# Kernel tuning notes

Measured on AMD Instinct MI355X. Metric: run time of the kernel, lower is better.

The kernel has to match this reference:

```python
import jax, jax.numpy as jnp
import numpy as np
import math

B, S, D, H, FF, L = 8, 1024, 1024, 8, 4096, 2
DK = D // H
NEG = -1e32
EPS = 1e-5


def _cosine_pe(seq_len, d_model):
    pos = jnp.arange(seq_len, dtype=jnp.float32)[:, None]
    div = jnp.exp(jnp.arange(0, d_model, 2, dtype=jnp.float32) * (-(math.log(10000.0) / d_model)))
    pe = jnp.zeros((seq_len, d_model), dtype=jnp.float32)
    pe = pe.at[:, 0::2].set(jnp.sin(pos * div))
    pe = pe.at[:, 1::2].set(jnp.cos(pos * div))
    return pe


def setup_inputs() -> dict:
    key = jax.random.key(0)
    ks = jax.random.split(key, 12)
    sc = 0.02
    g = lambda k, shape: (jax.random.normal(k, shape, jnp.float32) * sc)
    return {
        "q_embed": jax.random.normal(ks[0], (B, S, D), jnp.float32),
        "qa_embed": jax.random.normal(ks[1], (B, S, D), jnp.float32),
        "pos_emb": _cosine_pe(S, D),
        "Wk": g(ks[2], (L, D, D)), "bk": jnp.zeros((L, D), jnp.float32),
        "Wv": g(ks[3], (L, D, D)), "bv": jnp.zeros((L, D), jnp.float32),
        "Wo": g(ks[4], (L, D, D)), "bo": jnp.zeros((L, D), jnp.float32),
        "ln1_g": jnp.ones((L, D), jnp.float32), "ln1_b": jnp.zeros((L, D), jnp.float32),
        "W1": g(ks[5], (L, FF, D)), "b1": jnp.zeros((L, FF), jnp.float32),
        "W2": g(ks[6], (L, D, FF)), "b2": jnp.zeros((L, D), jnp.float32),
        "ln2_g": jnp.ones((L, D), jnp.float32), "ln2_b": jnp.zeros((L, D), jnp.float32),
    }


def _layernorm(x, g, b):
    m = jnp.mean(x, axis=-1, keepdims=True)
    v = jnp.mean(jnp.square(x - m), axis=-1, keepdims=True)
    return (x - m) * jax.lax.rsqrt(v + EPS) * g + b


def _mha(x, y, Wk, bk, Wv, bv, Wo, bo, allow):
    # kq_same=1: q and k both come from k_linear applied to x (query==key input)
    k = (jnp.einsum('bsd,od->bso', x, Wk) + bk).reshape(B, S, H, DK).transpose(0, 2, 1, 3)
    q = k  # identical projection and identical input
    v = (jnp.einsum('bsd,od->bso', y, Wv) + bv).reshape(B, S, H, DK).transpose(0, 2, 1, 3)
    scores = jnp.einsum('bhqd,bhkd->bhqk', q, k) / math.sqrt(DK)
    scores = jnp.where(allow, scores, NEG)  # masked_fill(mask==0, -1e32)
    attn = jax.nn.softmax(scores, axis=-1)
    attn = attn.at[:, :, 0, :].set(0.0)  # zero_pad: first query row zeroed
    out = jnp.einsum('bhqk,bhkd->bhqd', attn, v)
    out = out.transpose(0, 2, 1, 3).reshape(B, S, D)
    return jnp.einsum('bsd,od->bso', out, Wo) + bo


def reference(q_embed, qa_embed, pos_emb, Wk, bk, Wv, bv, Wo, bo,
              ln1_g, ln1_b, W1, b1, W2, b2, ln2_g, ln2_b):
    x = q_embed + pos_emb[None]
    y = qa_embed + pos_emb[None]
    # strictly-lower-triangular allowed positions (triu(k=0)==0)
    allow = jnp.tril(jnp.ones((S, S), dtype=bool), -1)[None, None]
    for l in range(L):
        q2 = _mha(x, x, y, Wk[l], bk[l], Wv[l], bv[l], Wo[l], bo[l], allow) if False else _mha(x, y, Wk[l], bk[l], Wv[l], bv[l], Wo[l], bo[l], allow)
        x = _layernorm(x + q2, ln1_g[l], ln1_b[l])
        ff = jnp.einsum('bsf,df->bsd', jax.nn.relu(jnp.einsum('bsd,fd->bsf', x, W1[l]) + b1[l]), W2[l]) + b2[l]
        x = _layernorm(x + ff, ln2_g[l], ln2_b[l])
    return x
```

## Files before the change

### kernel.cpp

```cpp
#include <hip/hip_runtime.h>
#include <hip/hip_bf16.h>
#include <cstdint>
#include <cstddef>

#define B_  8
#define S_  1024
#define D_  1024
#define H_  8
#define FF_ 4096
#define L_  2
#define DK_ 128

typedef __bf16 bf16x8 __attribute__((ext_vector_type(8)));
typedef float  f32x4  __attribute__((ext_vector_type(4)));

__device__ __forceinline__ unsigned short f2bf(float f) {
    union { float f; uint32_t u; } v; v.f = f;
    uint32_t r = v.u + 0x7fffu + ((v.u >> 16) & 1u);
    return (unsigned short)(r >> 16);
}
__device__ __forceinline__ float bf2f(unsigned short u) {
    union { uint32_t u; float f; } v; v.u = ((uint32_t)u) << 16; return v.f;
}

__global__ __launch_bounds__(256) void init_xy(
    const float* __restrict__ qe, const float* __restrict__ qa,
    const float* __restrict__ pe,
    unsigned short* __restrict__ xb, unsigned short* __restrict__ yb)
{
    int i = (blockIdx.x * 256 + threadIdx.x) * 4;
    int pi = i & (S_ * D_ - 1);
    float4 q = *(const float4*)(qe + i);
    float4 a = *(const float4*)(qa + i);
    float4 p = *(const float4*)(pe + pi);
    ushort4 xo; xo.x = f2bf(q.x + p.x); xo.y = f2bf(q.y + p.y);
    xo.z = f2bf(q.z + p.z); xo.w = f2bf(q.w + p.w);
    ushort4 yo; yo.x = f2bf(a.x + p.x); yo.y = f2bf(a.y + p.y);
    yo.z = f2bf(a.z + p.z); yo.w = f2bf(a.w + p.w);
    *(ushort4*)(xb + i) = xo;
    *(ushort4*)(yb + i) = yo;
}

__global__ __launch_bounds__(256) void cvt_bf16(
    const float* __restrict__ in, unsigned short* __restrict__ out)
{
    int i = (blockIdx.x * 256 + threadIdx.x) * 4;
    float4 f = *(const float4*)(in + i);
    ushort4 o; o.x = f2bf(f.x); o.y = f2bf(f.y); o.z = f2bf(f.z); o.w = f2bf(f.w);
    *(ushort4*)(out + i) = o;
}

template<bool RELU>
__global__ __launch_bounds__(512, 2) void gemm_bt8(
    const unsigned short* __restrict__ A, const unsigned short* __restrict__ W,
    const float* __restrict__ bias, unsigned short* __restrict__ Cout,
    int M, int N, int K)
{
    __shared__ unsigned short sA[2][256][64];
    __shared__ unsigned short sB[2][256][64];

    const int tid  = threadIdx.x;
    const int lane = tid & 63;
    const int w    = tid >> 6;
    const int l16  = lane & 15;
    const int quad = lane >> 4;
    const int wr   = w >> 2;
    const int wc   = w & 3;

    const int nwg = gridDim.x * gridDim.y;
    const int bid = blockIdx.y * gridDim.x + blockIdx.x;
    const int sb  = (bid & 7) * (nwg >> 3) + (bid >> 3);
    const int m0  = (sb / gridDim.x) * 256;
    const int n0  = (sb % gridDim.x) * 256;

    const int srow8 = lane >> 3;
    const int schk  = (lane & 7) ^ srow8;

    auto stA = [&](int i, int buf, int k0) {
        int r0 = i * 64 + w * 8;
        const unsigned short* g = A + (size_t)(m0 + r0 + srow8) * K + k0 + schk * 8;
        __builtin_amdgcn_global_load_lds(
            (const __attribute__((address_space(1))) unsigned int*)g,
            (__attribute__((address_space(3))) unsigned int*)&sA[buf][r0][0], 16, 0, 0);
    };
    auto stB = [&](int i, int buf, int k0) {
        int r0 = i * 64 + w * 8;
        const unsigned short* g = W + (size_t)(n0 + r0 + srow8) * K + k0 + schk * 8;
        __builtin_amdgcn_global_load_lds(
            (const __attribute__((address_space(1))) unsigned int*)g,
            (__attribute__((address_space(3))) unsigned int*)&sB[buf][r0][0], 16, 0, 0);
    };
    auto rdA = [&](int buf, int t, int ks) {
        int row = wr * 128 + t * 16 + l16;
        int chk = (ks * 4 + quad) ^ (row & 7);
        return *(const bf16x8*)&sA[buf][row][chk * 8];
    };
    auto rdB = [&](int buf, int j, int ks) {
        int row = wc * 64 + j * 16 + l16;
        int chk = (ks * 4 + quad) ^ (row & 7);
        return *(const bf16x8*)&sB[buf][row][chk * 8];
    };

    f32x4 acc[8][4] = {};
    const int NK = K >> 6;
    int cur = 0;

    stB(0, 0, 0); stB(1, 0, 0); stB(2, 0, 0); stB(3, 0, 0);
    stA(0, 0, 0); stA(2, 0, 0); stA(1, 0, 0); stA(3, 0, 0);
    asm volatile("s_waitcnt vmcnt(2)\n\ts_barrier" ::: "memory");

    for (int kt = 0; kt < NK; ++kt) {
        const bool pref = (kt + 1 < NK);
        const int  k1   = (kt + 1) << 6;
        const int  nb   = cur ^ 1;
        bf16x8 bfr[2][4];
        bf16x8 a0, a1, a2, a3;

        #pragma unroll
        for (int ks = 0; ks < 2; ++ks)
            #pragma unroll
            for (int j = 0; j < 4; ++j) bfr[ks][j] = rdB(cur, j, ks);
        a0 = rdA(cur, 0, 0); a1 = rdA(cur, 0, 1);
        a2 = rdA(cur, 1, 0); a3 = rdA(cur, 1, 1);
        if (pref) { stB(0, nb, k1); stB(1, nb, k1); }
        __builtin_amdgcn_s_setprio(1);
        #pragma unroll
        for (int j = 0; j < 4; ++j) {
            acc[0][j] = __builtin_amdgcn_mfma_f32_16x16x32_bf16(a0, bfr[0][j], acc[0][j], 0, 0, 0);
            acc[1][j] = __builtin_amdgcn_mfma_f32_16x16x32_bf16(a2, bfr[0][j], acc[1][j], 0, 0, 0);
        }
        #pragma unroll
        for (int j = 0; j < 4; ++j) {
            acc[0][j] = __builtin_amdgcn_mfma_f32_16x16x32_bf16(a1, bfr[1][j], acc[0][j], 0, 0, 0);
            acc[1][j] = __builtin_amdgcn_mfma_f32_16x16x32_bf16(a3, bfr[1][j], acc[1][j], 0, 0, 0);
        }
        __builtin_amdgcn_s_setprio(0);
        asm volatile("s_barrier" ::: "memory");

        a0 = rdA(cur, 2, 0); a1 = rdA(cur, 2, 1);
        a2 = rdA(cur, 3, 0); a3 = rdA(cur, 3, 1);
        if (pref) { stB(2, nb, k1); stB(3, nb, k1); }
        __builtin_amdgcn_s_setprio(1);
        #pragma unroll
        for (int j = 0; j < 4; ++j) {
            acc[2][j] = __builtin_amdgcn_mfma_f32_16x16x32_bf16(a0, bfr[0][j], acc[2][j], 0, 0, 0);
            acc[3][j] = __builtin_amdgcn_mfma_f32_16x16x32_bf16(a2, bfr[0][j], acc[3][j], 0, 0, 0);
        }
        #pragma unroll
        for (int j = 0; j < 4; ++j) {
            acc[2][j] = __builtin_amdgcn_mfma_f32_16x16x32_bf16(a1, bfr[1][j], acc[2][j], 0, 0, 0);
            acc[3][j] = __builtin_amdgcn_mfma_f32_16x16x32_bf16(a3, bfr[1][j], acc[3][j], 0, 0, 0);
        }
        __builtin_amdgcn_s_setprio(0);
        if (pref) asm volatile("s_waitcnt vmcnt(4)\n\ts_barrier" ::: "memory");
        else      asm volatile("s_waitcnt vmcnt(0)\n\ts_barrier" ::: "memory");

        a0 = rdA(cur, 4, 0); a1 = rdA(cur, 4, 1);
        a2 = rdA(cur, 5, 0); a3 = rdA(cur, 5, 1);
        if (pref) { stA(0, nb, k1); stA(2, nb, k1); }
        __builtin_amdgcn_s_setprio(1);
        #pragma unroll
        for (int j = 0; j < 4; ++j) {
            acc[4][j] = __builtin_amdgcn_mfma_f32_16x16x32_bf16(a0, bfr[0][j], acc[4][j], 0, 0, 0);
            acc[5][j] = __builtin_amdgcn_mfma_f32_16x16x32_bf16(a2, bfr[0][j], acc[5][j], 0, 0, 0);
        }
        #pragma unroll
        for (int j = 0; j < 4; ++j) {
            acc[4][j] = __builtin_amdgcn_mfma_f32_16x16x32_bf16(a1, bfr[1][j], acc[4][j], 0, 0, 0);
            acc[5][j] = __builtin_amdgcn_mfma_f32_16x16x32_bf16(a3, bfr[1][j], acc[5][j], 0, 0, 0);
        }
        __builtin_amdgcn_s_setprio(0);
        asm volatile("s_barrier" ::: "memory");

        a0 = rdA(cur, 6, 0); a1 = rdA(cur, 6, 1);
        a2 = rdA(cur, 7, 0); a3 = rdA(cur, 7, 1);
        if (pref) { stA(1, nb, k1); stA(3, nb, k1); }
        __builtin_amdgcn_s_setprio(1);
        #pragma unroll
        for (int j = 0; j < 4; ++j) {
            acc[6][j] = __builtin_amdgcn_mfma_f32_16x16x32_bf16(a0, bfr[0][j], acc[6][j], 0, 0, 0);
            acc[7][j] = __builtin_amdgcn_mfma_f32_16x16x32_bf16(a2, bfr[0][j], acc[7][j], 0, 0, 0);
        }
        #pragma unroll
        for (int j = 0; j < 4; ++j) {
            acc[6][j] = __builtin_amdgcn_mfma_f32_16x16x32_bf16(a1, bfr[1][j], acc[6][j], 0, 0, 0);
            acc[7][j] = __builtin_amdgcn_mfma_f32_16x16x32_bf16(a3, bfr[1][j], acc[7][j], 0, 0, 0);
        }
        __builtin_amdgcn_s_setprio(0);
        asm volatile("s_waitcnt vmcnt(2)\n\ts_barrier" ::: "memory");
        cur = nb;
    }

    #pragma unroll
    for (int t = 0; t < 8; ++t)
        #pragma unroll
        for (int j = 0; j < 4; ++j) {
            int row = m0 + wr * 128 + t * 16 + quad * 4;
            int col = n0 + wc * 64 + j * 16 + l16;
            float bcol = bias[col];
            #pragma unroll
            for (int r = 0; r < 4; ++r) {
                float v = acc[t][j][r] + bcol;
                if (RELU) v = fmaxf(v, 0.0f);
                Cout[(size_t)(row + r) * N + col] = f2bf(v);
            }
        }
}

template<int OMODE>
__global__ __launch_bounds__(512, 2) void gemm_btn(
    const unsigned short* __restrict__ A, const unsigned short* __restrict__ W,
    const float* __restrict__ bias, void* __restrict__ Cout,
    int M, int N, int K)
{
    __shared__ unsigned short sA[2][256][64];
    __shared__ unsigned short sB[2][128][64];

    const int tid  = threadIdx.x;
    const int lane = tid & 63;
    const int w    = tid >> 6;
    const int l16  = lane & 15;
    const int quad = lane >> 4;
    const int wr   = w >> 2;
    const int wc   = w & 3;

    const int nwg = gridDim.x * gridDim.y;
    const int bid = blockIdx.y * gridDim.x + blockIdx.x;
    const int sb  = (bid & 7) * (nwg >> 3) + (bid >> 3);
    const int m0  = (sb / gridDim.x) * 256;
    const int n0  = (sb % gridDim.x) * 128;

    const int srow8 = lane >> 3;
    const int schk  = (lane & 7) ^ srow8;

    auto stA = [&](int i, int buf, int k0) {
        int r0 = i * 64 + w * 8;
        const unsigned short* g = A + (size_t)(m0 + r0 + srow8) * K + k0 + schk * 8;
        __builtin_amdgcn_global_load_lds(
            (const __attribute__((address_space(1))) unsigned int*)g,
            (__attribute__((address_space(3))) unsigned int*)&sA[buf][r0][0], 16, 0, 0);
    };
    auto stB = [&](int i, int buf, int k0) {
        int r0 = i * 64 + w * 8;
        const unsigned short* g = W + (size_t)(n0 + r0 + srow8) * K + k0 + schk * 8;
        __builtin_amdgcn_global_load_lds(
            (const __attribute__((address_space(1))) unsigned int*)g,
            (__attribute__((address_space(3))) unsigned int*)&sB[buf][r0][0], 16, 0, 0);
    };
    auto rdA = [&](int buf, int t, int ks) {
        int row = wr * 128 + t * 16 + l16;
        int chk = (ks * 4 + quad) ^ (row & 7);
        return *(const bf16x8*)&sA[buf][row][chk * 8];
    };
    auto rdB = [&](int buf, int j, int ks) {
        int row = wc * 32 + j * 16 + l16;
        int chk = (ks * 4 + quad) ^ (row & 7);
        return *(const bf16x8*)&sB[buf][row][chk * 8];
    };

    f32x4 acc[8][2] = {};
    const int NK = K >> 6;
    int cur = 0;

    stB(0, 0, 0); stB(1, 0, 0);
    stA(0, 0, 0); stA(2, 0, 0);
    stA(1, 0, 0); stA(3, 0, 0);
    asm volatile("s_waitcnt vmcnt(2)\n\ts_barrier" ::: "memory");

    for (int kt = 0; kt < NK; ++kt) {
        const bool pref = (kt + 1 < NK);
        const int  k1   = (kt + 1) << 6;
        const int  nb   = cur ^ 1;
        bf16x8 bfr[2][2];
        bf16x8 a0, a1, a2, a3;

        #pragma unroll
        for (int ks = 0; ks < 2; ++ks)
            #pragma unroll
            for (int j = 0; j < 2; ++j) bfr[ks][j] = rdB(cur, j, ks);
        a0 = rdA(cur, 0, 0); a1 = rdA(cur, 0, 1);
        a2 = rdA(cur, 1, 0); a3 = rdA(cur, 1, 1);
        if (pref) { stB(0, nb, k1); stB(1, nb, k1); }
        __builtin_amdgcn_s_setprio(1);
        #pragma unroll
        for (int j = 0; j < 2; ++j) {
            acc[0][j] = __builtin_amdgcn_mfma_f32_16x16x32_bf16(a0, bfr[0][j], acc[0][j], 0, 0, 0);
            acc[1][j] = __builtin_amdgcn_mfma_f32_16x16x32_bf16(a2, bfr[0][j], acc[1][j], 0, 0, 0);
        }
        #pragma unroll
        for (int j = 0; j < 2; ++j) {
            acc[0][j] = __builtin_amdgcn_mfma_f32_16x16x32_bf16(a1, bfr[1][j], acc[0][j], 0, 0, 0);
            acc[1][j] = __builtin_amdgcn_mfma_f32_16x16x32_bf16(a3, bfr[1][j], acc[1][j], 0, 0, 0);
        }
        __builtin_amdgcn_s_setprio(0);
        asm volatile("s_barrier" ::: "memory");

        a0 = rdA(cur, 2, 0); a1 = rdA(cur, 2, 1);
        a2 = rdA(cur, 3, 0); a3 = rdA(cur, 3, 1);
        if (pref) { stA(0, nb, k1); stA(2, nb, k1); }
        __builtin_amdgcn_s_setprio(1);
        #pragma unroll
        for (int j = 0; j < 2; ++j) {
            acc[2][j] = __builtin_amdgcn_mfma_f32_16x16x32_bf16(a0, bfr[0][j], acc[2][j], 0, 0, 0);
            acc[3][j] = __builtin_amdgcn_mfma_f32_16x16x32_bf16(a2, bfr[0][j], acc[3][j], 0, 0, 0);
        }
        #pragma unroll
        for (int j = 0; j < 2; ++j) {
            acc[2][j] = __builtin_amdgcn_mfma_f32_16x16x32_bf16(a1, bfr[1][j], acc[2][j], 0, 0, 0);
            acc[3][j] = __builtin_amdgcn_mfma_f32_16x16x32_bf16(a3, bfr[1][j], acc[3][j], 0, 0, 0);
        }
        __builtin_amdgcn_s_setprio(0);
        if (pref) asm volatile("s_waitcnt vmcnt(4)\n\ts_barrier" ::: "memory");
        else      asm volatile("s_waitcnt vmcnt(0)\n\ts_barrier" ::: "memory");

        a0 = rdA(cur, 4, 0); a1 = rdA(cur, 4, 1);
        a2 = rdA(cur, 5, 0); a3 = rdA(cur, 5, 1);
        if (pref) { stA(1, nb, k1); stA(3, nb, k1); }
        __builtin_amdgcn_s_setprio(1);
        #pragma unroll
        for (int j = 0; j < 2; ++j) {
            acc[4][j] = __builtin_amdgcn_mfma_f32_16x16x32_bf16(a0, bfr[0][j], acc[4][j], 0, 0, 0);
            acc[5][j] = __builtin_amdgcn_mfma_f32_16x16x32_bf16(a2, bfr[0][j], acc[5][j], 0, 0, 0);
        }
        #pragma unroll
        for (int j = 0; j < 2; ++j) {
            acc[4][j] = __builtin_amdgcn_mfma_f32_16x16x32_bf16(a1, bfr[1][j], acc[4][j], 0, 0, 0);
            acc[5][j] = __builtin_amdgcn_mfma_f32_16x16x32_bf16(a3, bfr[1][j], acc[5][j], 0, 0, 0);
        }
        __builtin_amdgcn_s_setprio(0);
        asm volatile("s_barrier" ::: "memory");

        a0 = rdA(cur, 6, 0); a1 = rdA(cur, 6, 1);
        a2 = rdA(cur, 7, 0); a3 = rdA(cur, 7, 1);
        __builtin_amdgcn_s_setprio(1);
        #pragma unroll
        for (int j = 0; j < 2; ++j) {
            acc[6][j] = __builtin_amdgcn_mfma_f32_16x16x32_bf16(a0, bfr[0][j], acc[6][j], 0, 0, 0);
            acc[7][j] = __builtin_amdgcn_mfma_f32_16x16x32_bf16(a2, bfr[0][j], acc[7][j], 0, 0, 0);
        }
        #pragma unroll
        for (int j = 0; j < 2; ++j) {
            acc[6][j] = __builtin_amdgcn_mfma_f32_16x16x32_bf16(a1, bfr[1][j], acc[6][j], 0, 0, 0);
            acc[7][j] = __builtin_amdgcn_mfma_f32_16x16x32_bf16(a3, bfr[1][j], acc[7][j], 0, 0, 0);
        }
        __builtin_amdgcn_s_setprio(0);
        asm volatile("s_waitcnt vmcnt(2)\n\ts_barrier" ::: "memory");
        cur = nb;
    }

    #pragma unroll
    for (int t = 0; t < 8; ++t)
        #pragma unroll
        for (int j = 0; j < 2; ++j) {
            int row = m0 + wr * 128 + t * 16 + quad * 4;
            int col = n0 + wc * 32 + j * 16 + l16;
            float bcol = bias[col];
            float v[4];
            #pragma unroll
            for (int r = 0; r < 4; ++r) v[r] = acc[t][j][r] + bcol;
            if (OMODE == 1) {
                #pragma unroll
                for (int r = 0; r < 4; ++r)
                    ((unsigned short*)Cout)[(size_t)(row + r) * N + col] = f2bf(v[r]);
            } else {
                int key = row & (S_ - 1);
                int bb  = row >> 10;
                int hh  = col >> 7, dim = col & (DK_ - 1);
                unsigned short* dst = (unsigned short*)Cout
                    + ((size_t)(bb * H_ + hh) * DK_ + dim) * S_ + key;
                ushort4 o4; o4.x = f2bf(v[0]); o4.y = f2bf(v[1]);
                o4.z = f2bf(v[2]); o4.w = f2bf(v[3]);
                *(ushort4*)dst = o4;
            }
        }
}

__global__ __launch_bounds__(256) void attn_mfma(
    const unsigned short* __restrict__ Kbuf, const unsigned short* __restrict__ Vtbuf,
    unsigned short* __restrict__ Obuf)
{
    __shared__ unsigned short sK[2][64][128];
    __shared__ unsigned short sVt[2][128][64];
    __shared__ unsigned short sP[4][16][72];

    const int tid  = threadIdx.x;
    const int lane = tid & 63;
    const int w    = tid >> 6;
    const int l16  = lane & 15;
    const int quad = lane >> 4;
    const int pa   = blockIdx.x;
    const int bh   = blockIdx.y;
    const int b    = bh >> 3, h = bh & 7;
    const unsigned short* KB  = Kbuf  + ((size_t)b * S_) * D_ + h * DK_;
    const unsigned short* VTB = Vtbuf + (size_t)bh * DK_ * S_;

    const float scale = 0.08838834764831845f;

    auto stage = [&](int kt, int buf) {
        #pragma unroll
        for (int i = 0; i < 4; ++i) {
            int r0  = w * 16 + i * 4;
            int row = r0 + (lane >> 4);
            int c   = (lane & 15) ^ (row & 15);
            const unsigned short* g = KB + (size_t)(kt * 64 + row) * D_ + c * 8;
            __builtin_amdgcn_global_load_lds(
                (const __attribute__((address_space(1))) unsigned int*)g,
                (__attribute__((address_space(3))) unsigned int*)&sK[buf][r0][0], 16, 0, 0);
        }
        #pragma unroll
        for (int i = 0; i < 4; ++i) {
            int r0  = w * 32 + i * 8;
            int row = r0 + (lane >> 3);
            int c   = (lane & 7) ^ (row & 7);
            const unsigned short* g = VTB + (size_t)row * S_ + kt * 64 + c * 8;
            __builtin_amdgcn_global_load_lds(
                (const __attribute__((address_space(1))) unsigned int*)g,
                (__attribute__((address_space(3))) unsigned int*)&sVt[buf][r0][0], 16, 0, 0);
        }
    };

    #pragma unroll
    for (int half = 0; half < 2; ++half) {
        const int qt = half == 0 ? (15 - pa) : pa;
        const int q0 = qt * 64;

        bf16x8 qf[4];
        {
            const unsigned short* qrow = KB + (size_t)(q0 + w * 16 + l16) * D_ + quad * 8;
            #pragma unroll
            for (int ks = 0; ks < 4; ++ks)
                qf[ks] = *(const bf16x8*)(qrow + ks * 32);
        }

        f32x4 Oacc[8] = {};
        float m_run[4] = {-1e30f, -1e30f, -1e30f, -1e30f};
        float l_run[4] = {};

        int cur = 0;
        stage(0, cur);

        for (int kt = 0; kt <= qt; ++kt) {
            __syncthreads();
            if (kt < qt) stage(kt + 1, cur ^ 1);

            f32x4 sacc[4];
            #pragma unroll
            for (int nt = 0; nt < 4; ++nt) {
                f32x4 a = {};
                #pragma unroll
                for (int ks = 0; ks < 4; ++ks) {
                    int kr = nt * 16 + l16;
                    int p  = (ks * 4 + quad) ^ (kr & 15);
                    bf16x8 kf = *(const bf16x8*)&sK[cur][kr][p * 8];
                    a = __builtin_amdgcn_mfma_f32_16x16x32_bf16(qf[ks], kf, a, 0, 0, 0);
                }
                sacc[nt] = a;
            }

            const bool diag = (kt == qt);
            #pragma unroll
            for (int nt = 0; nt < 4; ++nt)
                #pragma unroll
                for (int r = 0; r < 4; ++r) {
                    float v = sacc[nt][r] * scale;
                    if (diag) {
                        int nidx = nt * 16 + l16;
                        int midx = w * 16 + quad * 4 + r;
                        if (nidx >= midx) v = -1e30f;
                    }
                    sacc[nt][r] = v;
                }

            float alpha[4];
            #pragma unroll
            for (int r = 0; r < 4; ++r) {
                float mx = fmaxf(fmaxf(sacc[0][r], sacc[1][r]), fmaxf(sacc[2][r], sacc[3][r]));
                mx = fmaxf(mx, __shfl_xor(mx, 1));
                mx = fmaxf(mx, __shfl_xor(mx, 2));
                mx = fmaxf(mx, __shfl_xor(mx, 4));
                mx = fmaxf(mx, __shfl_xor(mx, 8));
                float mn = fmaxf(m_run[r], mx);
                alpha[r] = __expf(m_run[r] - mn);
                m_run[r] = mn;
            }
            #pragma unroll
            for (int r = 0; r < 4; ++r) {
                float rs = 0.0f;
                #pragma unroll
                for (int nt = 0; nt < 4; ++nt) {
                    float e = __expf(sacc[nt][r] - m_run[r]);
                    sacc[nt][r] = e;
                    rs += e;
                }
                rs += __shfl_xor(rs, 1);
                rs += __shfl_xor(rs, 2);
                rs += __shfl_xor(rs, 4);
                rs += __shfl_xor(rs, 8);
                l_run[r] = l_run[r] * alpha[r] + rs;
            }
            #pragma unroll
            for (int o = 0; o < 8; ++o)
                #pragma unroll
                for (int r = 0; r < 4; ++r)
                    Oacc[o][r] *= alpha[r];

            #pragma unroll
            for (int nt = 0; nt < 4; ++nt)
                #pragma unroll
                for (int r = 0; r < 4; ++r)
                    sP[w][quad * 4 + r][nt * 16 + l16] = f2bf(sacc[nt][r]);

            bf16x8 pf[2];
            #pragma unroll
            for (int ks = 0; ks < 2; ++ks)
                pf[ks] = *(const bf16x8*)&sP[w][l16][ks * 32 + quad * 8];
            #pragma unroll
            for (int nt = 0; nt < 8; ++nt) {
                #pragma unroll
                for (int ks = 0; ks < 2; ++ks) {
                    int vr = nt * 16 + l16;
                    int p  = (ks * 4 + quad) ^ (vr & 7);
                    bf16x8 vf = *(const bf16x8*)&sVt[cur][vr][p * 8];
                    Oacc[nt] = __builtin_amdgcn_mfma_f32_16x16x32_bf16(pf[ks], vf, Oacc[nt], 0, 0, 0);
                }
            }
            cur ^= 1;
        }

        float inv[4];
        #pragma unroll
        for (int r = 0; r < 4; ++r) {
            int m = q0 + w * 16 + quad * 4 + r;
            inv[r] = (l_run[r] > 0.0f && m != 0) ? 1.0f / l_run[r] : 0.0f;
        }
        #pragma unroll
        for (int nt = 0; nt < 8; ++nt)
            #pragma unroll
            for (int r = 0; r < 4; ++r) {
                int m = q0 + w * 16 + quad * 4 + r;
                Obuf[((size_t)b * S_ + m) * D_ + h * DK_ + nt * 16 + l16] =
                    f2bf(Oacc[nt][r] * inv[r]);
            }
    }
}

template<bool FINAL>
__global__ __launch_bounds__(256) void ln_res(
    const unsigned short* __restrict__ xin, const unsigned short* __restrict__ delta,
    const float* __restrict__ g, const float* __restrict__ bta,
    unsigned short* __restrict__ xbout, float* __restrict__ fout)
{
    __shared__ float red1[4], red2[4];
    const int row = blockIdx.x;
    const int tid = threadIdx.x;
    const int c = tid * 4;
    ushort4 xu = *(const ushort4*)(xin + (size_t)row * D_ + c);
    ushort4 du = *(const ushort4*)(delta + (size_t)row * D_ + c);
    float t0 = bf2f(xu.x) + bf2f(du.x), t1 = bf2f(xu.y) + bf2f(du.y);
    float t2 = bf2f(xu.z) + bf2f(du.z), t3 = bf2f(xu.w) + bf2f(du.w);

    float s = t0 + t1 + t2 + t3;
    #pragma unroll
    for (int off = 32; off > 0; off >>= 1) s += __shfl_down(s, off);
    if ((tid & 63) == 0) red1[tid >> 6] = s;
    __syncthreads();
    float mean = (red1[0] + red1[1] + red1[2] + red1[3]) * (1.0f / 1024.0f);

    float e0 = t0 - mean, e1 = t1 - mean, e2 = t2 - mean, e3 = t3 - mean;
    float ss = e0 * e0 + e1 * e1 + e2 * e2 + e3 * e3;
    #pragma unroll
    for (int off = 32; off > 0; off >>= 1) ss += __shfl_down(ss, off);
    if ((tid & 63) == 0) red2[tid >> 6] = ss;
    __syncthreads();
    float var = (red2[0] + red2[1] + red2[2] + red2[3]) * (1.0f / 1024.0f);
    float rstd = rsqrtf(var + 1e-5f);

    float4 gv = *(const float4*)(g + c);
    float4 bv = *(const float4*)(bta + c);
    float o0 = e0 * rstd * gv.x + bv.x;
    float o1 = e1 * rstd * gv.y + bv.y;
    float o2 = e2 * rstd * gv.z + bv.z;
    float o3 = e3 * rstd * gv.w + bv.w;
    if (FINAL) {
        *(float4*)(fout + (size_t)row * D_ + c) = make_float4(o0, o1, o2, o3);
    } else {
        ushort4 ob; ob.x = f2bf(o0); ob.y = f2bf(o1); ob.z = f2bf(o2); ob.w = f2bf(o3);
        *(ushort4*)(xbout + (size_t)row * D_ + c) = ob;
    }
}

extern "C" void kernel_launch(void* const* d_in, const int* in_sizes, int n_in,
                              void* d_out, int out_size, void* d_ws, size_t ws_size,
                              hipStream_t stream)
{
    const float* qe   = (const float*)d_in[0];
    const float* qa   = (const float*)d_in[1];
    const float* pe   = (const float*)d_in[2];
    const float* Wk   = (const float*)d_in[3];
    const float* bk   = (const float*)d_in[4];
    const float* Wv   = (const float*)d_in[5];
    const float* bv   = (const float*)d_in[6];
    const float* Wo   = (const float*)d_in[7];
    const float* bo   = (const float*)d_in[8];
    const float* ln1g = (const float*)d_in[9];
    const float* ln1b = (const float*)d_in[10];
    const float* W1   = (const float*)d_in[11];
    const float* b1   = (const float*)d_in[12];
    const float* W2   = (const float*)d_in[13];
    const float* b2   = (const float*)d_in[14];
    const float* ln2g = (const float*)d_in[15];
    const float* ln2b = (const float*)d_in[16];

    const size_t BSD = (size_t)B_ * S_ * D_;
    const size_t BSF = (size_t)B_ * S_ * FF_;
    const size_t WDD = (size_t)D_ * D_;
    const size_t WFD = (size_t)FF_ * D_;

    char* p = (char*)d_ws;
    auto take = [&](size_t bytes) { char* r = p; p += (bytes + 255) & ~255ULL; return r; };
    unsigned short* xb    = (unsigned short*)take(BSD * 2);
    unsigned short* yb    = (unsigned short*)take(BSD * 2);
    unsigned short* delta = (unsigned short*)take(BSD * 2);
    char*           uni   = take(BSF * 2);
    unsigned short* Kb    = (unsigned short*)uni;
    unsigned short* Vt    = Kb + BSD;
    unsigned short* attnb = Vt + BSD;
    unsigned short* hb    = (unsigned short*)uni;
    unsigned short* wslot = (unsigned short*)take(WFD * 2);

    init_xy<<<(int)(BSD / 4 / 256), 256, 0, stream>>>(qe, qa, pe, xb, yb);

    const int M = B_ * S_;
    for (int l = 0; l < L_; ++l) {
        cvt_bf16<<<(int)(WDD / 1024), 256, 0, stream>>>(Wk + l * WDD, wslot);
        gemm_btn<1><<<dim3(D_ / 128, M / 256), 512, 0, stream>>>(
            xb, wslot, bk + l * D_, Kb, M, D_, D_);
        cvt_bf16<<<(int)(WDD / 1024), 256, 0, stream>>>(Wv + l * WDD, wslot);
        gemm_btn<2><<<dim3(D_ / 128, M / 256), 512, 0, stream>>>(
            yb, wslot, bv + l * D_, Vt, M, D_, D_);
        attn_mfma<<<dim3(8, B_ * H_), 256, 0, stream>>>(Kb, Vt, attnb);
        cvt_bf16<<<(int)(WDD / 1024), 256, 0, stream>>>(Wo + l * WDD, wslot);
        gemm_btn<1><<<dim3(D_ / 128, M / 256), 512, 0, stream>>>(
            attnb, wslot, bo + l * D_, delta, M, D_, D_);
        ln_res<false><<<M, 256, 0, stream>>>(xb, delta, ln1g + l * D_, ln1b + l * D_, xb, nullptr);
        cvt_bf16<<<(int)(WFD / 1024), 256, 0, stream>>>(W1 + l * WFD, wslot);
        gemm_bt8<true><<<dim3(FF_ / 256, M / 256), 512, 0, stream>>>(
            xb, wslot, b1 + l * FF_, hb, M, FF_, D_);
        cvt_bf16<<<(int)(WFD / 1024), 256, 0, stream>>>(W2 + l * WFD, wslot);
        gemm_btn<1><<<dim3(D_ / 128, M / 256), 512, 0, stream>>>(
            hb, wslot, b2 + l * D_, delta, M, D_, FF_);
        if (l == L_ - 1)
            ln_res<true><<<M, 256, 0, stream>>>(xb, delta, ln2g + l * D_, ln2b + l * D_,
                                               nullptr, (float*)d_out);
        else
            ln_res<false><<<M, 256, 0, stream>>>(xb, delta, ln2g + l * D_, ln2b + l * D_,
                                                xb, nullptr);
    }
}
```

Baseline: 872.5 us.

## Add split-K FFN2 GEMM with fused partial-sum LayerNorm and simpler 128x128 GEMM

Replaces the heavily hand-scheduled 256x128 N=1024 GEMM with a simpler 128x128 tile kernel using 256 threads, which gives more workgroups for the D-output projections. The FF2 GEMM (K=4096) becomes a split-K-by-2 kernel on 256x256 tiles that writes fp32 partials. The following LayerNorm sums both partials plus the bias, so no separate reduction pass is needed. The split-K path costs extra fp32 write and read traffic and only runs when the workspace is large enough, and the simpler GEMM loses the interleaved prefetch scheduling.

```diff
diff --git a/kernel.cpp b/kernel.cpp
--- a/kernel.cpp
+++ b/kernel.cpp
@@ -50,314 +50,89 @@
     *(ushort4*)(out + i) = o;
 }
 
-template<bool RELU>
-__global__ __launch_bounds__(512, 2) void gemm_bt8(
+template<bool RELU, int OMODE>
+__global__ __launch_bounds__(256) void gemm_bt(
     const unsigned short* __restrict__ A, const unsigned short* __restrict__ W,
-    const float* __restrict__ bias, unsigned short* __restrict__ Cout,
+    const float* __restrict__ bias, void* __restrict__ Cout,
     int M, int N, int K)
 {
-    __shared__ unsigned short sA[2][256][64];
-    __shared__ unsigned short sB[2][256][64];
+    __shared__ unsigned short sA[2][128][64];
+    __shared__ unsigned short sW[2][128][64];
 
     const int tid  = threadIdx.x;
     const int lane = tid & 63;
     const int w    = tid >> 6;
     const int l16  = lane & 15;
     const int quad = lane >> 4;
-    const int wr   = w >> 2;
-    const int wc   = w & 3;
-
-    const int nwg = gridDim.x * gridDim.y;
-    const int bid = blockIdx.y * gridDim.x + blockIdx.x;
-    const int sb  = (bid & 7) * (nwg >> 3) + (bid >> 3);
-    const int m0  = (sb / gridDim.x) * 256;
-    const int n0  = (sb % gridDim.x) * 256;
-
-    const int srow8 = lane >> 3;
-    const int schk  = (lane & 7) ^ srow8;
-
-    auto stA = [&](int i, int buf, int k0) {
-        int r0 = i * 64 + w * 8;
-        const unsigned short* g = A + (size_t)(m0 + r0 + srow8) * K + k0 + schk * 8;
-        __builtin_amdgcn_global_load_lds(
-            (const __attribute__((address_space(1))) unsigned int*)g,
-            (__attribute__((address_space(3))) unsigned int*)&sA[buf][r0][0], 16, 0, 0);
-    };
-    auto stB = [&](int i, int buf, int k0) {
-        int r0 = i * 64 + w * 8;
-        const unsigned short* g = W + (size_t)(n0 + r0 + srow8) * K + k0 + schk * 8;
-        __builtin_amdgcn_global_load_lds(
-            (const __attribute__((address_space(1))) unsigned int*)g,
-            (__attribute__((address_space(3))) unsigned int*)&sB[buf][r0][0], 16, 0, 0);
-    };
-    auto rdA = [&](int buf, int t, int ks) {
-        int row = wr * 128 + t * 16 + l16;
-        int chk = (ks * 4 + quad) ^ (row & 7);
-        return *(const bf16x8*)&sA[buf][row][chk * 8];
-    };
-    auto rdB = [&](int buf, int j, int ks) {
-        int row = wc * 64 + j * 16 + l16;
-        int chk = (ks * 4 + quad) ^ (row & 7);
-        return *(const bf16x8*)&sB[buf][row][chk * 8];
-    };
-
-    f32x4 acc[8][4] = {};
+    const int m0 = blockIdx.y * 128;
+    const int n0 = blockIdx.x * 128;
+    const int rw = (w >> 1) * 64;
+    const int cw = (w & 1) * 64;
+
+    const int srow   = lane >> 3;
+    const int schunk = lane & 7;
+
+    auto stage = [&](int k0, int buf) {
+        #pragma unroll
+        for (int i = 0; i < 4; ++i) {
+            int r0  = w * 32 + i * 8;
+            int row = r0 + srow;
+            int gc  = schunk ^ (row & 7);
+            const unsigned short* ga = A + (size_t)(m0 + row) * K + k0 + gc * 8;
+            const unsigned short* gw = W + (size_t)(n0 + row) * K + k0 + gc * 8;
+            __builtin_amdgcn_global_load_lds(
+                (const __attribute__((address_space(1))) unsigned int*)ga,
+                (__attribute__((address_space(3))) unsigned int*)&sA[buf][r0][0], 16, 0, 0);
+            __builtin_amdgcn_global_load_lds(
+                (const __attribute__((address_space(1))) unsigned int*)gw,
+                (__attribute__((address_space(3))) unsigned int*)&sW[buf][r0][0], 16, 0, 0);
+        }
+    };
+
+    f32x4 acc[4][4] = {};
     const int NK = K >> 6;
     int cur = 0;
-
-    stB(0, 0, 0); stB(1, 0, 0); stB(2, 0, 0); stB(3, 0, 0);
-    stA(0, 0, 0); stA(2, 0, 0); stA(1, 0, 0); stA(3, 0, 0);
-    asm volatile("s_waitcnt vmcnt(2)\n\ts_barrier" ::: "memory");
+    stage(0, 0);
 
     for (int kt = 0; kt < NK; ++kt) {
-        const bool pref = (kt + 1 < NK);
-        const int  k1   = (kt + 1) << 6;
-        const int  nb   = cur ^ 1;
-        bf16x8 bfr[2][4];
-        bf16x8 a0, a1, a2, a3;
-
-        #pragma unroll
-        for (int ks = 0; ks < 2; ++ks)
-            #pragma unroll
-            for (int j = 0; j < 4; ++j) bfr[ks][j] = rdB(cur, j, ks);
-        a0 = rdA(cur, 0, 0); a1 = rdA(cur, 0, 1);
-        a2 = rdA(cur, 1, 0); a3 = rdA(cur, 1, 1);
-        if (pref) { stB(0, nb, k1); stB(1, nb, k1); }
-        __builtin_amdgcn_s_setprio(1);
-        #pragma unroll
-        for (int j = 0; j < 4; ++j) {
-            acc[0][j] = __builtin_amdgcn_mfma_f32_16x16x32_bf16(a0, bfr[0][j], acc[0][j], 0, 0, 0);
-            acc[1][j] = __builtin_amdgcn_mfma_f32_16x16x32_bf16(a2, bfr[0][j], acc[1][j], 0, 0, 0);
-        }
-        #pragma unroll
-        for (int j = 0; j < 4; ++j) {
-            acc[0][j] = __builtin_amdgcn_mfma_f32_16x16x32_bf16(a1, bfr[1][j], acc[0][j], 0, 0, 0);
-            acc[1][j] = __builtin_amdgcn_mfma_f32_16x16x32_bf16(a3, bfr[1][j], acc[1][j], 0, 0, 0);
-        }
-        __builtin_amdgcn_s_setprio(0);
-        asm volatile("s_barrier" ::: "memory");
-
-        a0 = rdA(cur, 2, 0); a1 = rdA(cur, 2, 1);
-        a2 = rdA(cur, 3, 0); a3 = rdA(cur, 3, 1);
-        if (pref) { stB(2, nb, k1); stB(3, nb, k1); }
-        __builtin_amdgcn_s_setprio(1);
-        #pragma unroll
-        for (int j = 0; j < 4; ++j) {
-            acc[2][j] = __builtin_amdgcn_mfma_f32_16x16x32_bf16(a0, bfr[0][j], acc[2][j], 0, 0, 0);
-            acc[3][j] = __builtin_amdgcn_mfma_f32_16x16x32_bf16(a2, bfr[0][j], acc[3][j], 0, 0, 0);
-        }
-        #pragma unroll
-        for (int j = 0; j < 4; ++j) {
-            acc[2][j] = __builtin_amdgcn_mfma_f32_16x16x32_bf16(a1, bfr[1][j], acc[2][j], 0, 0, 0);
-            acc[3][j] = __builtin_amdgcn_mfma_f32_16x16x32_bf16(a3, bfr[1][j], acc[3][j], 0, 0, 0);
-        }
-        __builtin_amdgcn_s_setprio(0);
-        if (pref) asm volatile("s_waitcnt vmcnt(4)\n\ts_barrier" ::: "memory");
-        else      asm volatile("s_waitcnt vmcnt(0)\n\ts_barrier" ::: "memory");
-
-        a0 = rdA(cur, 4, 0); a1 = rdA(cur, 4, 1);
-        a2 = rdA(cur, 5, 0); a3 = rdA(cur, 5, 1);
-        if (pref) { stA(0, nb, k1); stA(2, nb, k1); }
-        __builtin_amdgcn_s_setprio(1);
-        #pragma unroll
-        for (int j = 0; j < 4; ++j) {
-            acc[4][j] = __builtin_amdgcn_mfma_f32_16x16x32_bf16(a0, bfr[0][j], acc[4][j], 0, 0, 0);
-            acc[5][j] = __builtin_amdgcn_mfma_f32_16x16x32_bf16(a2, bfr[0][j], acc[5][j], 0, 0, 0);
-        }
-        #pragma unroll
-        for (int j = 0; j < 4; ++j) {
-            acc[4][j] = __builtin_amdgcn_mfma_f32_16x16x32_bf16(a1, bfr[1][j], acc[4][j], 0, 0, 0);
-            acc[5][j] = __builtin_amdgcn_mfma_f32_16x16x32_bf16(a3, bfr[1][j], acc[5][j], 0, 0, 0);
-        }
-        __builtin_amdgcn_s_setprio(0);
-        asm volatile("s_barrier" ::: "memory");
-
-        a0 = rdA(cur, 6, 0); a1 = rdA(cur, 6, 1);
-        a2 = rdA(cur, 7, 0); a3 = rdA(cur, 7, 1);
-        if (pref) { stA(1, nb, k1); stA(3, nb, k1); }
-        __builtin_amdgcn_s_setprio(1);
-        #pragma unroll
-        for (int j = 0; j < 4; ++j) {
-            acc[6][j] = __builtin_amdgcn_mfma_f32_16x16x32_bf16(a0, bfr[0][j], acc[6][j], 0, 0, 0);
-            acc[7][j] = __builtin_amdgcn_mfma_f32_16x16x32_bf16(a2, bfr[0][j], acc[7][j], 0, 0, 0);
-        }
-        #pragma unroll
-        for (int j = 0; j < 4; ++j) {
-            acc[6][j] = __builtin_amdgcn_mfma_f32_16x16x32_bf16(a1, bfr[1][j], acc[6][j], 0, 0, 0);
-            acc[7][j] = __builtin_amdgcn_mfma_f32_16x16x32_bf16(a3, bfr[1][j], acc[7][j], 0, 0, 0);
-        }
-        __builtin_amdgcn_s_setprio(0);
-        asm volatile("s_waitcnt vmcnt(2)\n\ts_barrier" ::: "memory");
-        cur = nb;
+        __syncthreads();
+        if (kt + 1 < NK) stage((kt + 1) << 6, cur ^ 1);
+
+        #pragma unroll
+        for (int ks = 0; ks < 2; ++ks) {
+            bf16x8 af[4], wf[4];
+            #pragma unroll
+            for (int t = 0; t < 4; ++t) {
+                int arow = rw + t * 16 + l16;
+                int achk = (ks * 4 + quad) ^ (arow & 7);
+                af[t] = *(const bf16x8*)&sA[cur][arow][achk * 8];
+                int wrow = cw + t * 16 + l16;
+                int wchk = (ks * 4 + quad) ^ (wrow & 7);
+                wf[t] = *(const bf16x8*)&sW[cur][wrow][wchk * 8];
+            }
+            #pragma unroll
+            for (int it = 0; it < 4; ++it)
+                #pragma unroll
+                for (int jt = 0; jt < 4; ++jt)
+                    acc[it][jt] = __builtin_amdgcn_mfma_f32_16x16x32_bf16(
+                        af[it], wf[jt], acc[it][jt], 0, 0, 0);
+        }
+        cur ^= 1;
     }
 
     #pragma unroll
-    for (int t = 0; t < 8; ++t)
-        #pragma unroll
-        for (int j = 0; j < 4; ++j) {
-            int row = m0 + wr * 128 + t * 16 + quad * 4;
-            int col = n0 + wc * 64 + j * 16 + l16;
-            float bcol = bias[col];
-            #pragma unroll
-            for (int r = 0; r < 4; ++r) {
-                float v = acc[t][j][r] + bcol;
-                if (RELU) v = fmaxf(v, 0.0f);
-                Cout[(size_t)(row + r) * N + col] = f2bf(v);
-            }
-        }
-}
-
-template<int OMODE>
-__global__ __launch_bounds__(512, 2) void gemm_btn(
-    const unsigned short* __restrict__ A, const unsigned short* __restrict__ W,
-    const float* __restrict__ bias, void* __restrict__ Cout,
-    int M, int N, int K)
-{
-    __shared__ unsigned short sA[2][256][64];
-    __shared__ unsigned short sB[2][128][64];
-
-    const int tid  = threadIdx.x;
-    const int lane = tid & 63;
-    const int w    = tid >> 6;
-    const int l16  = lane & 15;
-    const int quad = lane >> 4;
-    const int wr   = w >> 2;
-    const int wc   = w & 3;
-
-    const int nwg = gridDim.x * gridDim.y;
-    const int bid = blockIdx.y * gridDim.x + blockIdx.x;
-    const int sb  = (bid & 7) * (nwg >> 3) + (bid >> 3);
-    const int m0  = (sb / gridDim.x) * 256;
-    const int n0  = (sb % gridDim.x) * 128;
-
-    const int srow8 = lane >> 3;
-    const int schk  = (lane & 7) ^ srow8;
-
-    auto stA = [&](int i, int buf, int k0) {
-        int r0 = i * 64 + w * 8;
-        const unsigned short* g = A + (size_t)(m0 + r0 + srow8) * K + k0 + schk * 8;
-        __builtin_amdgcn_global_load_lds(
-            (const __attribute__((address_space(1))) unsigned int*)g,
-            (__attribute__((address_space(3))) unsigned int*)&sA[buf][r0][0], 16, 0, 0);
-    };
-    auto stB = [&](int i, int buf, int k0) {
-        int r0 = i * 64 + w * 8;
-        const unsigned short* g = W + (size_t)(n0 + r0 + srow8) * K + k0 + schk * 8;
-        __builtin_amdgcn_global_load_lds(
-            (const __attribute__((address_space(1))) unsigned int*)g,
-            (__attribute__((address_space(3))) unsigned int*)&sB[buf][r0][0], 16, 0, 0);
-    };
-    auto rdA = [&](int buf, int t, int ks) {
-        int row = wr * 128 + t * 16 + l16;
-        int chk = (ks * 4 + quad) ^ (row & 7);
-        return *(const bf16x8*)&sA[buf][row][chk * 8];
-    };
-    auto rdB = [&](int buf, int j, int ks) {
-        int row = wc * 32 + j * 16 + l16;
-        int chk = (ks * 4 + quad) ^ (row & 7);
-        return *(const bf16x8*)&sB[buf][row][chk * 8];
-    };
-
-    f32x4 acc[8][2] = {};
-    const int NK = K >> 6;
-    int cur = 0;
-
-    stB(0, 0, 0); stB(1, 0, 0);
-    stA(0, 0, 0); stA(2, 0, 0);
-    stA(1, 0, 0); stA(3, 0, 0);
-    asm volatile("s_waitcnt vmcnt(2)\n\ts_barrier" ::: "memory");
-
-    for (int kt = 0; kt < NK; ++kt) {
-        const bool pref = (kt + 1 < NK);
-        const int  k1   = (kt + 1) << 6;
-        const int  nb   = cur ^ 1;
-        bf16x8 bfr[2][2];
-        bf16x8 a0, a1, a2, a3;
-
-        #pragma unroll
-        for (int ks = 0; ks < 2; ++ks)
-            #pragma unroll
-            for (int j = 0; j < 2; ++j) bfr[ks][j] = rdB(cur, j, ks);
-        a0 = rdA(cur, 0, 0); a1 = rdA(cur, 0, 1);
-        a2 = rdA(cur, 1, 0); a3 = rdA(cur, 1, 1);
-        if (pref) { stB(0, nb, k1); stB(1, nb, k1); }
-        __builtin_amdgcn_s_setprio(1);
-        #pragma unroll
-        for (int j = 0; j < 2; ++j) {
-            acc[0][j] = __builtin_amdgcn_mfma_f32_16x16x32_bf16(a0, bfr[0][j], acc[0][j], 0, 0, 0);
-            acc[1][j] = __builtin_amdgcn_mfma_f32_16x16x32_bf16(a2, bfr[0][j], acc[1][j], 0, 0, 0);
-        }
-        #pragma unroll
-        for (int j = 0; j < 2; ++j) {
-            acc[0][j] = __builtin_amdgcn_mfma_f32_16x16x32_bf16(a1, bfr[1][j], acc[0][j], 0, 0, 0);
-            acc[1][j] = __builtin_amdgcn_mfma_f32_16x16x32_bf16(a3, bfr[1][j], acc[1][j], 0, 0, 0);
-        }
-        __builtin_amdgcn_s_setprio(0);
-        asm volatile("s_barrier" ::: "memory");
-
-        a0 = rdA(cur, 2, 0); a1 = rdA(cur, 2, 1);
-        a2 = rdA(cur, 3, 0); a3 = rdA(cur, 3, 1);
-        if (pref) { stA(0, nb, k1); stA(2, nb, k1); }
-        __builtin_amdgcn_s_setprio(1);
-        #pragma unroll
-        for (int j = 0; j < 2; ++j) {
-            acc[2][j] = __builtin_amdgcn_mfma_f32_16x16x32_bf16(a0, bfr[0][j], acc[2][j], 0, 0, 0);
-            acc[3][j] = __builtin_amdgcn_mfma_f32_16x16x32_bf16(a2, bfr[0][j], acc[3][j], 0, 0, 0);
-        }
-        #pragma unroll
-        for (int j = 0; j < 2; ++j) {
-            acc[2][j] = __builtin_amdgcn_mfma_f32_16x16x32_bf16(a1, bfr[1][j], acc[2][j], 0, 0, 0);
-            acc[3][j] = __builtin_amdgcn_mfma_f32_16x16x32_bf16(a3, bfr[1][j], acc[3][j], 0, 0, 0);
-        }
-        __builtin_amdgcn_s_setprio(0);
-        if (pref) asm volatile("s_waitcnt vmcnt(4)\n\ts_barrier" ::: "memory");
-        else      asm volatile("s_waitcnt vmcnt(0)\n\ts_barrier" ::: "memory");
-
-        a0 = rdA(cur, 4, 0); a1 = rdA(cur, 4, 1);
-        a2 = rdA(cur, 5, 0); a3 = rdA(cur, 5, 1);
-        if (pref) { stA(1, nb, k1); stA(3, nb, k1); }
-        __builtin_amdgcn_s_setprio(1);
-        #pragma unroll
-        for (int j = 0; j < 2; ++j) {
-            acc[4][j] = __builtin_amdgcn_mfma_f32_16x16x32_bf16(a0, bfr[0][j], acc[4][j], 0, 0, 0);
-            acc[5][j] = __builtin_amdgcn_mfma_f32_16x16x32_bf16(a2, bfr[0][j], acc[5][j], 0, 0, 0);
-        }
-        #pragma unroll
-        for (int j = 0; j < 2; ++j) {
-            acc[4][j] = __builtin_amdgcn_mfma_f32_16x16x32_bf16(a1, bfr[1][j], acc[4][j], 0, 0, 0);
-            acc[5][j] = __builtin_amdgcn_mfma_f32_16x16x32_bf16(a3, bfr[1][j], acc[5][j], 0, 0, 0);
-        }
-        __builtin_amdgcn_s_setprio(0);
-        asm volatile("s_barrier" ::: "memory");
-
-        a0 = rdA(cur, 6, 0); a1 = rdA(cur, 6, 1);
-        a2 = rdA(cur, 7, 0); a3 = rdA(cur, 7, 1);
-        __builtin_amdgcn_s_setprio(1);
-        #pragma unroll
-        for (int j = 0; j < 2; ++j) {
-            acc[6][j] = __builtin_amdgcn_mfma_f32_16x16x32_bf16(a0, bfr[0][j], acc[6][j], 0, 0, 0);
-            acc[7][j] = __builtin_amdgcn_mfma_f32_16x16x32_bf16(a2, bfr[0][j], acc[7][j], 0, 0, 0);
-        }
-        #pragma unroll
-        for (int j = 0; j < 2; ++j) {
-            acc[6][j] = __builtin_amdgcn_mfma_f32_16x16x32_bf16(a1, bfr[1][j], acc[6][j], 0, 0, 0);
-            acc[7][j] = __builtin_amdgcn_mfma_f32_16x16x32_bf16(a3, bfr[1][j], acc[7][j], 0, 0, 0);
-        }
-        __builtin_amdgcn_s_setprio(0);
-        asm volatile("s_waitcnt vmcnt(2)\n\ts_barrier" ::: "memory");
-        cur = nb;
-    }
-
-    #pragma unroll
-    for (int t = 0; t < 8; ++t)
-        #pragma unroll
-        for (int j = 0; j < 2; ++j) {
-            int row = m0 + wr * 128 + t * 16 + quad * 4;
-            int col = n0 + wc * 32 + j * 16 + l16;
+    for (int it = 0; it < 4; ++it)
+        #pragma unroll
+        for (int jt = 0; jt < 4; ++jt) {
+            int row = m0 + rw + it * 16 + quad * 4;
+            int col = n0 + cw + jt * 16 + l16;
             float bcol = bias[col];
             float v[4];
             #pragma unroll
-            for (int r = 0; r < 4; ++r) v[r] = acc[t][j][r] + bcol;
+            for (int r = 0; r < 4; ++r) {
+                v[r] = acc[it][jt][r] + bcol;
+                if (RELU) v[r] = fmaxf(v[r], 0.0f);
+            }
             if (OMODE == 1) {
                 #pragma unroll
                 for (int r = 0; r < 4; ++r)
@@ -375,6 +150,316 @@
         }
 }
 
+template<bool RELU>
+__global__ __launch_bounds__(512, 2) void gemm_bt8(
+    const unsigned short* __restrict__ A, const unsigned short* __restrict__ W,
+    const float* __restrict__ bias, unsigned short* __restrict__ Cout,
+    int M, int N, int K)
+{
+    __shared__ unsigned short sA[2][256][64];
+    __shared__ unsigned short sB[2][256][64];
+
+    const int tid  = threadIdx.x;
+    const int lane = tid & 63;
+    const int w    = tid >> 6;
+    const int l16  = lane & 15;
+    const int quad = lane >> 4;
+    const int wr   = w >> 2;
+    const int wc   = w & 3;
+
+    const int nwg = gridDim.x * gridDim.y;
+    const int bid = blockIdx.y * gridDim.x + blockIdx.x;
+    const int sb  = (bid & 7) * (nwg >> 3) + (bid >> 3);
+    const int m0  = (sb / gridDim.x) * 256;
+    const int n0  = (sb % gridDim.x) * 256;
+
+    const int srow8 = lane >> 3;
+    const int schk  = (lane & 7) ^ srow8;
+
+    auto stA = [&](int i, int buf, int k0) {
+        int r0 = i * 64 + w * 8;
+        const unsigned short* g = A + (size_t)(m0 + r0 + srow8) * K + k0 + schk * 8;
+        __builtin_amdgcn_global_load_lds(
+            (const __attribute__((address_space(1))) unsigned int*)g,
+            (__attribute__((address_space(3))) unsigned int*)&sA[buf][r0][0], 16, 0, 0);
+    };
+    auto stB = [&](int i, int buf, int k0) {
+        int r0 = i * 64 + w * 8;
+        const unsigned short* g = W + (size_t)(n0 + r0 + srow8) * K + k0 + schk * 8;
+        __builtin_amdgcn_global_load_lds(
+            (const __attribute__((address_space(1))) unsigned int*)g,
+            (__attribute__((address_space(3))) unsigned int*)&sB[buf][r0][0], 16, 0, 0);
+    };
+    auto rdA = [&](int buf, int t, int ks) {
+        int row = wr * 128 + t * 16 + l16;
+        int chk = (ks * 4 + quad) ^ (row & 7);
+        return *(const bf16x8*)&sA[buf][row][chk * 8];
+    };
+    auto rdB = [&](int buf, int j, int ks) {
+        int row = wc * 64 + j * 16 + l16;
+        int chk = (ks * 4 + quad) ^ (row & 7);
+        return *(const bf16x8*)&sB[buf][row][chk * 8];
+    };
+
+    f32x4 acc[8][4] = {};
+    const int NK = K >> 6;
+    int cur = 0;
+
+    stB(0, 0, 0); stB(1, 0, 0); stB(2, 0, 0); stB(3, 0, 0);
+    stA(0, 0, 0); stA(2, 0, 0); stA(1, 0, 0); stA(3, 0, 0);
+    asm volatile("s_waitcnt vmcnt(2)\n\ts_barrier" ::: "memory");
+
+    for (int kt = 0; kt < NK; ++kt) {
+        const bool pref = (kt + 1 < NK);
+        const int  k1   = (kt + 1) << 6;
+        const int  nb   = cur ^ 1;
+        bf16x8 bfr[2][4];
+        bf16x8 a0, a1, a2, a3;
+
+        #pragma unroll
+        for (int ks = 0; ks < 2; ++ks)
+            #pragma unroll
+            for (int j = 0; j < 4; ++j) bfr[ks][j] = rdB(cur, j, ks);
+        a0 = rdA(cur, 0, 0); a1 = rdA(cur, 0, 1);
+        a2 = rdA(cur, 1, 0); a3 = rdA(cur, 1, 1);
+        if (pref) { stB(0, nb, k1); stB(1, nb, k1); }
+        __builtin_amdgcn_s_setprio(1);
+        #pragma unroll
+        for (int j = 0; j < 4; ++j) {
+            acc[0][j] = __builtin_amdgcn_mfma_f32_16x16x32_bf16(a0, bfr[0][j], acc[0][j], 0, 0, 0);
+            acc[1][j] = __builtin_amdgcn_mfma_f32_16x16x32_bf16(a2, bfr[0][j], acc[1][j], 0, 0, 0);
+        }
+        #pragma unroll
+        for (int j = 0; j < 4; ++j) {
+            acc[0][j] = __builtin_amdgcn_mfma_f32_16x16x32_bf16(a1, bfr[1][j], acc[0][j], 0, 0, 0);
+            acc[1][j] = __builtin_amdgcn_mfma_f32_16x16x32_bf16(a3, bfr[1][j], acc[1][j], 0, 0, 0);
+        }
+        __builtin_amdgcn_s_setprio(0);
+        asm volatile("s_barrier" ::: "memory");
+
+        a0 = rdA(cur, 2, 0); a1 = rdA(cur, 2, 1);
+        a2 = rdA(cur, 3, 0); a3 = rdA(cur, 3, 1);
+        if (pref) { stB(2, nb, k1); stB(3, nb, k1); }
+        __builtin_amdgcn_s_setprio(1);
+        #pragma unroll
+        for (int j = 0; j < 4; ++j) {
+            acc[2][j] = __builtin_amdgcn_mfma_f32_16x16x32_bf16(a0, bfr[0][j], acc[2][j], 0, 0, 0);
+            acc[3][j] = __builtin_amdgcn_mfma_f32_16x16x32_bf16(a2, bfr[0][j], acc[3][j], 0, 0, 0);
+        }
+        #pragma unroll
+        for (int j = 0; j < 4; ++j) {
+            acc[2][j] = __builtin_amdgcn_mfma_f32_16x16x32_bf16(a1, bfr[1][j], acc[2][j], 0, 0, 0);
+            acc[3][j] = __builtin_amdgcn_mfma_f32_16x16x32_bf16(a3, bfr[1][j], acc[3][j], 0, 0, 0);
+        }
+        __builtin_amdgcn_s_setprio(0);
+        if (pref) asm volatile("s_waitcnt vmcnt(4)\n\ts_barrier" ::: "memory");
+        else      asm volatile("s_waitcnt vmcnt(0)\n\ts_barrier" ::: "memory");
+
+        a0 = rdA(cur, 4, 0); a1 = rdA(cur, 4, 1);
+        a2 = rdA(cur, 5, 0); a3 = rdA(cur, 5, 1);
+        if (pref) { stA(0, nb, k1); stA(2, nb, k1); }
+        __builtin_amdgcn_s_setprio(1);
+        #pragma unroll
+        for (int j = 0; j < 4; ++j) {
+            acc[4][j] = __builtin_amdgcn_mfma_f32_16x16x32_bf16(a0, bfr[0][j], acc[4][j], 0, 0, 0);
+            acc[5][j] = __builtin_amdgcn_mfma_f32_16x16x32_bf16(a2, bfr[0][j], acc[5][j], 0, 0, 0);
+        }
+        #pragma unroll
+        for (int j = 0; j < 4; ++j) {
+            acc[4][j] = __builtin_amdgcn_mfma_f32_16x16x32_bf16(a1, bfr[1][j], acc[4][j], 0, 0, 0);
+            acc[5][j] = __builtin_amdgcn_mfma_f32_16x16x32_bf16(a3, bfr[1][j], acc[5][j], 0, 0, 0);
+        }
+        __builtin_amdgcn_s_setprio(0);
+        asm volatile("s_barrier" ::: "memory");
+
+        a0 = rdA(cur, 6, 0); a1 = rdA(cur, 6, 1);
+        a2 = rdA(cur, 7, 0); a3 = rdA(cur, 7, 1);
+        if (pref) { stA(1, nb, k1); stA(3, nb, k1); }
+        __builtin_amdgcn_s_setprio(1);
+        #pragma unroll
+        for (int j = 0; j < 4; ++j) {
+            acc[6][j] = __builtin_amdgcn_mfma_f32_16x16x32_bf16(a0, bfr[0][j], acc[6][j], 0, 0, 0);
+            acc[7][j] = __builtin_amdgcn_mfma_f32_16x16x32_bf16(a2, bfr[0][j], acc[7][j], 0, 0, 0);
+        }
+        #pragma unroll
+        for (int j = 0; j < 4; ++j) {
+            acc[6][j] = __builtin_amdgcn_mfma_f32_16x16x32_bf16(a1, bfr[1][j], acc[6][j], 0, 0, 0);
+            acc[7][j] = __builtin_amdgcn_mfma_f32_16x16x32_bf16(a3, bfr[1][j], acc[7][j], 0, 0, 0);
+        }
+        __builtin_amdgcn_s_setprio(0);
+        asm volatile("s_waitcnt vmcnt(2)\n\ts_barrier" ::: "memory");
+        cur = nb;
+    }
+
+    #pragma unroll
+    for (int t = 0; t < 8; ++t)
+        #pragma unroll
+        for (int j = 0; j < 4; ++j) {
+            int row = m0 + wr * 128 + t * 16 + quad * 4;
+            int col = n0 + wc * 64 + j * 16 + l16;
+            float bcol = bias[col];
+            #pragma unroll
+            for (int r = 0; r < 4; ++r) {
+                float v = acc[t][j][r] + bcol;
+                if (RELU) v = fmaxf(v, 0.0f);
+                Cout[(size_t)(row + r) * N + col] = f2bf(v);
+            }
+        }
+}
+
+__global__ __launch_bounds__(512, 2) void gemm_sk(
+    const unsigned short* __restrict__ A, const unsigned short* __restrict__ W,
+    float* __restrict__ P, int M, int N, int K, int Kh)
+{
+    __shared__ unsigned short sA[2][256][64];
+    __shared__ unsigned short sB[2][256][64];
+
+    const int tid  = threadIdx.x;
+    const int lane = tid & 63;
+    const int w    = tid >> 6;
+    const int l16  = lane & 15;
+    const int quad = lane >> 4;
+    const int wr   = w >> 2;
+    const int wc   = w & 3;
+
+    const int nwg = gridDim.x * gridDim.y;
+    const int bid = blockIdx.y * gridDim.x + blockIdx.x;
+    const int sb  = (bid & 7) * (nwg >> 3) + (bid >> 3);
+    const int m0  = (sb / gridDim.x) * 256;
+    const int n0  = (sb % gridDim.x) * 256;
+    const int kb  = blockIdx.z * Kh;
+    P += (size_t)blockIdx.z * M * N;
+
+    const int srow8 = lane >> 3;
+    const int schk  = (lane & 7) ^ srow8;
+
+    auto stA = [&](int i, int buf, int k0) {
+        int r0 = i * 64 + w * 8;
+        const unsigned short* g = A + (size_t)(m0 + r0 + srow8) * K + k0 + schk * 8;
+        __builtin_amdgcn_global_load_lds(
+            (const __attribute__((address_space(1))) unsigned int*)g,
+            (__attribute__((address_space(3))) unsigned int*)&sA[buf][r0][0], 16, 0, 0);
+    };
+    auto stB = [&](int i, int buf, int k0) {
+        int r0 = i * 64 + w * 8;
+        const unsigned short* g = W + (size_t)(n0 + r0 + srow8) * K + k0 + schk * 8;
+        __builtin_amdgcn_global_load_lds(
+            (const __attribute__((address_space(1))) unsigned int*)g,
+            (__attribute__((address_space(3))) unsigned int*)&sB[buf][r0][0], 16, 0, 0);
+    };
+    auto rdA = [&](int buf, int t, int ks) {
+        int row = wr * 128 + t * 16 + l16;
+        int chk = (ks * 4 + quad) ^ (row & 7);
+        return *(const bf16x8*)&sA[buf][row][chk * 8];
+    };
+    auto rdB = [&](int buf, int j, int ks) {
+        int row = wc * 64 + j * 16 + l16;
+        int chk = (ks * 4 + quad) ^ (row & 7);
+        return *(const bf16x8*)&sB[buf][row][chk * 8];
+    };
+
+    f32x4 acc[8][4] = {};
+    const int NK = Kh >> 6;
+    int cur = 0;
+
+    stB(0, 0, kb); stB(1, 0, kb); stB(2, 0, kb); stB(3, 0, kb);
+    stA(0, 0, kb); stA(2, 0, kb); stA(1, 0, kb); stA(3, 0, kb);
+    asm volatile("s_waitcnt vmcnt(2)\n\ts_barrier" ::: "memory");
+
+    for (int kt = 0; kt < NK; ++kt) {
+        const bool pref = (kt + 1 < NK);
+        const int  k1   = kb + ((kt + 1) << 6);
+        const int  nb   = cur ^ 1;
+        bf16x8 bfr[2][4];
+        bf16x8 a0, a1, a2, a3;
+
+        #pragma unroll
+        for (int ks = 0; ks < 2; ++ks)
+            #pragma unroll
+            for (int j = 0; j < 4; ++j) bfr[ks][j] = rdB(cur, j, ks);
+        a0 = rdA(cur, 0, 0); a1 = rdA(cur, 0, 1);
+        a2 = rdA(cur, 1, 0); a3 = rdA(cur, 1, 1);
+        if (pref) { stB(0, nb, k1); stB(1, nb, k1); }
+        __builtin_amdgcn_s_setprio(1);
+        #pragma unroll
+        for (int j = 0; j < 4; ++j) {
+            acc[0][j] = __builtin_amdgcn_mfma_f32_16x16x32_bf16(a0, bfr[0][j], acc[0][j], 0, 0, 0);
+            acc[1][j] = __builtin_amdgcn_mfma_f32_16x16x32_bf16(a2, bfr[0][j], acc[1][j], 0, 0, 0);
+        }
+        #pragma unroll
+        for (int j = 0; j < 4; ++j) {
+            acc[0][j] = __builtin_amdgcn_mfma_f32_16x16x32_bf16(a1, bfr[1][j], acc[0][j], 0, 0, 0);
+            acc[1][j] = __builtin_amdgcn_mfma_f32_16x16x32_bf16(a3, bfr[1][j], acc[1][j], 0, 0, 0);
+        }
+        __builtin_amdgcn_s_setprio(0);
+        asm volatile("s_barrier" ::: "memory");
+
+        a0 = rdA(cur, 2, 0); a1 = rdA(cur, 2, 1);
+        a2 = rdA(cur, 3, 0); a3 = rdA(cur, 3, 1);
+        if (pref) { stB(2, nb, k1); stB(3, nb, k1); }
+        __builtin_amdgcn_s_setprio(1);
+        #pragma unroll
+        for (int j = 0; j < 4; ++j) {
+            acc[2][j] = __builtin_amdgcn_mfma_f32_16x16x32_bf16(a0, bfr[0][j], acc[2][j], 0, 0, 0);
+            acc[3][j] = __builtin_amdgcn_mfma_f32_16x16x32_bf16(a2, bfr[0][j], acc[3][j], 0, 0, 0);
+        }
+        #pragma unroll
+        for (int j = 0; j < 4; ++j) {
+            acc[2][j] = __builtin_amdgcn_mfma_f32_16x16x32_bf16(a1, bfr[1][j], acc[2][j], 0, 0, 0);
+            acc[3][j] = __builtin_amdgcn_mfma_f32_16x16x32_bf16(a3, bfr[1][j], acc[3][j], 0, 0, 0);
+        }
+        __builtin_amdgcn_s_setprio(0);
+        if (pref) asm volatile("s_waitcnt vmcnt(4)\n\ts_barrier" ::: "memory");
+        else      asm volatile("s_waitcnt vmcnt(0)\n\ts_barrier" ::: "memory");
+
+        a0 = rdA(cur, 4, 0); a1 = rdA(cur, 4, 1);
+        a2 = rdA(cur, 5, 0); a3 = rdA(cur, 5, 1);
+        if (pref) { stA(0, nb, k1); stA(2, nb, k1); }
+        __builtin_amdgcn_s_setprio(1);
+        #pragma unroll
+        for (int j = 0; j < 4; ++j) {
+            acc[4][j] = __builtin_amdgcn_mfma_f32_16x16x32_bf16(a0, bfr[0][j], acc[4][j], 0, 0, 0);
+            acc[5][j] = __builtin_amdgcn_mfma_f32_16x16x32_bf16(a2, bfr[0][j], acc[5][j], 0, 0, 0);
+        }
+        #pragma unroll
+        for (int j = 0; j < 4; ++j) {
+            acc[4][j] = __builtin_amdgcn_mfma_f32_16x16x32_bf16(a1, bfr[1][j], acc[4][j], 0, 0, 0);
+            acc[5][j] = __builtin_amdgcn_mfma_f32_16x16x32_bf16(a3, bfr[1][j], acc[5][j], 0, 0, 0);
+        }
+        __builtin_amdgcn_s_setprio(0);
+        asm volatile("s_barrier" ::: "memory");
+
+        a0 = rdA(cur, 6, 0); a1 = rdA(cur, 6, 1);
+        a2 = rdA(cur, 7, 0); a3 = rdA(cur, 7, 1);
+        if (pref) { stA(1, nb, k1); stA(3, nb, k1); }
+        __builtin_amdgcn_s_setprio(1);
+        #pragma unroll
+        for (int j = 0; j < 4; ++j) {
+            acc[6][j] = __builtin_amdgcn_mfma_f32_16x16x32_bf16(a0, bfr[0][j], acc[6][j], 0, 0, 0);
+            acc[7][j] = __builtin_amdgcn_mfma_f32_16x16x32_bf16(a2, bfr[0][j], acc[7][j], 0, 0, 0);
+        }
+        #pragma unroll
+        for (int j = 0; j < 4; ++j) {
+            acc[6][j] = __builtin_amdgcn_mfma_f32_16x16x32_bf16(a1, bfr[1][j], acc[6][j], 0, 0, 0);
+            acc[7][j] = __builtin_amdgcn_mfma_f32_16x16x32_bf16(a3, bfr[1][j], acc[7][j], 0, 0, 0);
+        }
+        __builtin_amdgcn_s_setprio(0);
+        asm volatile("s_waitcnt vmcnt(2)\n\ts_barrier" ::: "memory");
+        cur = nb;
+    }
+
+    #pragma unroll
+    for (int t = 0; t < 8; ++t)
+        #pragma unroll
+        for (int j = 0; j < 4; ++j) {
+            int row = m0 + wr * 128 + t * 16 + quad * 4;
+            int col = n0 + wc * 64 + j * 16 + l16;
+            #pragma unroll
+            for (int r = 0; r < 4; ++r)
+                P[(size_t)(row + r) * N + col] = acc[t][j][r];
+        }
+}
+
 __global__ __launch_bounds__(256) void attn_mfma(
     const unsigned short* __restrict__ Kbuf, const unsigned short* __restrict__ Vtbuf,
     unsigned short* __restrict__ Obuf)
@@ -558,6 +643,57 @@
     ushort4 du = *(const ushort4*)(delta + (size_t)row * D_ + c);
     float t0 = bf2f(xu.x) + bf2f(du.x), t1 = bf2f(xu.y) + bf2f(du.y);
     float t2 = bf2f(xu.z) + bf2f(du.z), t3 = bf2f(xu.w) + bf2f(du.w);
+
+    float s = t0 + t1 + t2 + t3;
+    #pragma unroll
+    for (int off = 32; off > 0; off >>= 1) s += __shfl_down(s, off);
+    if ((tid & 63) == 0) red1[tid >> 6] = s;
+    __syncthreads();
+    float mean = (red1[0] + red1[1] + red1[2] + red1[3]) * (1.0f / 1024.0f);
+
+    float e0 = t0 - mean, e1 = t1 - mean, e2 = t2 - mean, e3 = t3 - mean;
+    float ss = e0 * e0 + e1 * e1 + e2 * e2 + e3 * e3;
+    #pragma unroll
+    for (int off = 32; off > 0; off >>= 1) ss += __shfl_down(ss, off);
+    if ((tid & 63) == 0) red2[tid >> 6] = ss;
+    __syncthreads();
+    float var = (red2[0] + red2[1] + red2[2] + red2[3]) * (1.0f / 1024.0f);
+    float rstd = rsqrtf(var + 1e-5f);
+
+    float4 gv = *(const float4*)(g + c);
+    float4 bv = *(const float4*)(bta + c);
+    float o0 = e0 * rstd * gv.x + bv.x;
+    float o1 = e1 * rstd * gv.y + bv.y;
+    float o2 = e2 * rstd * gv.z + bv.z;
+    float o3 = e3 * rstd * gv.w + bv.w;
+    if (FINAL) {
+        *(float4*)(fout + (size_t)row * D_ + c) = make_float4(o0, o1, o2, o3);
+    } else {
+        ushort4 ob; ob.x = f2bf(o0); ob.y = f2bf(o1); ob.z = f2bf(o2); ob.w = f2bf(o3);
+        *(ushort4*)(xbout + (size_t)row * D_ + c) = ob;
+    }
+}
+
+template<bool FINAL>
+__global__ __launch_bounds__(256) void ln_res_sk(
+    const unsigned short* __restrict__ xin,
+    const float* __restrict__ p0, const float* __restrict__ p1,
+    const float* __restrict__ wbias,
+    const float* __restrict__ g, const float* __restrict__ bta,
+    unsigned short* __restrict__ xbout, float* __restrict__ fout)
+{
+    __shared__ float red1[4], red2[4];
+    const int row = blockIdx.x;
+    const int tid = threadIdx.x;
+    const int c = tid * 4;
+    ushort4 xu = *(const ushort4*)(xin + (size_t)row * D_ + c);
+    float4 a0 = *(const float4*)(p0 + (size_t)row * D_ + c);
+    float4 a1 = *(const float4*)(p1 + (size_t)row * D_ + c);
+    float4 wb = *(const float4*)(wbias + c);
+    float t0 = bf2f(xu.x) + a0.x + a1.x + wb.x;
+    float t1 = bf2f(xu.y) + a0.y + a1.y + wb.y;
+    float t2 = bf2f(xu.z) + a0.z + a1.z + wb.z;
+    float t3 = bf2f(xu.w) + a0.w + a1.w + wb.w;
 
     float s = t0 + t1 + t2 + t3;
     #pragma unroll
@@ -628,32 +764,49 @@
     unsigned short* hb    = (unsigned short*)uni;
     unsigned short* wslot = (unsigned short*)take(WFD * 2);
 
+    const size_t base_used = (size_t)(p - (char*)d_ws);
+    const bool   use_sk    = ws_size >= base_used + BSD * 8 + 256;
+    float* pbuf = use_sk ? (float*)take(BSD * 8) : nullptr;
+
     init_xy<<<(int)(BSD / 4 / 256), 256, 0, stream>>>(qe, qa, pe, xb, yb);
 
     const int M = B_ * S_;
     for (int l = 0; l < L_; ++l) {
         cvt_bf16<<<(int)(WDD / 1024), 256, 0, stream>>>(Wk + l * WDD, wslot);
-        gemm_btn<1><<<dim3(D_ / 128, M / 256), 512, 0, stream>>>(
+        gemm_bt<false, 1><<<dim3(D_ / 128, M / 128), 256, 0, stream>>>(
             xb, wslot, bk + l * D_, Kb, M, D_, D_);
         cvt_bf16<<<(int)(WDD / 1024), 256, 0, stream>>>(Wv + l * WDD, wslot);
-        gemm_btn<2><<<dim3(D_ / 128, M / 256), 512, 0, stream>>>(
+        gemm_bt<false, 2><<<dim3(D_ / 128, M / 128), 256, 0, stream>>>(
             yb, wslot, bv + l * D_, Vt, M, D_, D_);
         attn_mfma<<<dim3(8, B_ * H_), 256, 0, stream>>>(Kb, Vt, attnb);
         cvt_bf16<<<(int)(WDD / 1024), 256, 0, stream>>>(Wo + l * WDD, wslot);
-        gemm_btn<1><<<dim3(D_ / 128, M / 256), 512, 0, stream>>>(
+        gemm_bt<false, 1><<<dim3(D_ / 128, M / 128), 256, 0, stream>>>(
             attnb, wslot, bo + l * D_, delta, M, D_, D_);
         ln_res<false><<<M, 256, 0, stream>>>(xb, delta, ln1g + l * D_, ln1b + l * D_, xb, nullptr);
         cvt_bf16<<<(int)(WFD / 1024), 256, 0, stream>>>(W1 + l * WFD, wslot);
         gemm_bt8<true><<<dim3(FF_ / 256, M / 256), 512, 0, stream>>>(
             xb, wslot, b1 + l * FF_, hb, M, FF_, D_);
         cvt_bf16<<<(int)(WFD / 1024), 256, 0, stream>>>(W2 + l * WFD, wslot);
-        gemm_btn<1><<<dim3(D_ / 128, M / 256), 512, 0, stream>>>(
-            hb, wslot, b2 + l * D_, delta, M, D_, FF_);
-        if (l == L_ - 1)
-            ln_res<true><<<M, 256, 0, stream>>>(xb, delta, ln2g + l * D_, ln2b + l * D_,
-                                               nullptr, (float*)d_out);
-        else
-            ln_res<false><<<M, 256, 0, stream>>>(xb, delta, ln2g + l * D_, ln2b + l * D_,
-                                                xb, nullptr);
+        if (use_sk) {
+            gemm_sk<<<dim3(D_ / 256, M / 256, 2), 512, 0, stream>>>(
+                hb, wslot, pbuf, M, D_, FF_, FF_ / 2);
+            if (l == L_ - 1)
+                ln_res_sk<true><<<M, 256, 0, stream>>>(
+                    xb, pbuf, pbuf + BSD, b2 + l * D_,
+                    ln2g + l * D_, ln2b + l * D_, nullptr, (float*)d_out);
+            else
+                ln_res_sk<false><<<M, 256, 0, stream>>>(
+                    xb, pbuf, pbuf + BSD, b2 + l * D_,
+                    ln2g + l * D_, ln2b + l * D_, xb, nullptr);
+        } else {
+            gemm_bt<false, 1><<<dim3(D_ / 128, M / 128), 256, 0, stream>>>(
+                hb, wslot, b2 + l * D_, delta, M, D_, FF_);
+            if (l == L_ - 1)
+                ln_res<true><<<M, 256, 0, stream>>>(xb, delta, ln2g + l * D_, ln2b + l * D_,
+                                                   nullptr, (float*)d_out);
+            else
+                ln_res<false><<<M, 256, 0, stream>>>(xb, delta, ln2g + l * D_, ln2b + l * D_,
+                                                    xb, nullptr);
+        }
     }
 }
```

New measurement: 798.7 us. -8.5%, faster.
